# Optimization experiments

Measured on AMD Instinct MI355X. Metric: run time of the kernel, lower is better.

## Reference

```python
import jax, jax.numpy as jnp
import numpy as np

N = 4096     # batch of positions
E = 32       # descriptor buckets (experts)
NBLK = 12    # residual blocks per head


def _ln(x, g, b, eps=1e-5):
    m = x.mean(-1, keepdims=True)
    v = ((x - m) ** 2).mean(-1, keepdims=True)
    return (x - m) / jnp.sqrt(v + eps) * g + b


def _gelu(x):
    return jax.nn.gelu(x, approximate=False)  # torch nn.GELU default = exact erf


def setup_inputs() -> dict:
    key = jax.random.key(0)
    ks = iter(jax.random.split(key, 64))

    def nrm(shape, scale=0.05):
        return jax.random.normal(next(ks), shape, jnp.float32) * scale

    return {
        "piece_idx": jax.random.randint(next(ks), (N, 64), 0, 12),
        "side_flag": jax.random.randint(next(ks), (N,), 0, 2),
        "ep_file": jax.random.randint(next(ks), (N,), 0, 8),
        "castle_ms": jax.random.uniform(next(ks), (N, 4), jnp.float32),
        "fifty_a": jax.random.uniform(next(ks), (N,), jnp.float32),
        "descriptor_index": jax.random.randint(next(ks), (N,), 0, E),
        # per-bucket embedding tables, stacked on a leading expert axis
        "Wp_w": nrm((E, 64, 12, 32)), "Wp_b": nrm((E, 64, 12, 32)),
        "Wc_w": nrm((E, 4, 32)), "Wc_b": nrm((E, 4, 32)),
        "Wep_w": nrm((E, 8, 32)), "Wep_b": nrm((E, 8, 32)),
        "Wf_w": nrm((E, 2, 32)), "Wf_b": nrm((E, 2, 32)),
        # per-bucket MLP head params (weights stored as [in,out])
        "fc1_w": nrm((E, 2240, 256)), "fc1_b": nrm((E, 256)),
        "ln1_g": jnp.ones((E, 256)), "ln1_b": jnp.zeros((E, 256)),
        "fc2_w": nrm((E, 256, 32)), "fc2_b": nrm((E, 32)),
        "ln2_g": jnp.ones((E, 32)), "ln2_b": jnp.zeros((E, 32)),
        "blkA_w": nrm((NBLK, E, 32, 32)), "blkA_b": nrm((NBLK, E, 32)),
        "blkA_g": jnp.ones((NBLK, E, 32)), "blkA_be": jnp.zeros((NBLK, E, 32)),
        "blkB_w": nrm((NBLK, E, 32, 32)), "blkB_b": nrm((NBLK, E, 32)),
        "blkB_g": jnp.ones((NBLK, E, 32)), "blkB_be": jnp.zeros((NBLK, E, 32)),
        "out_w": nrm((E, 32, 51)), "out_b": nrm((E, 51)),
        "bins": jnp.linspace(0.0, 1.0, 51),
    }


def reference(piece_idx, side_flag, ep_file, castle_ms, fifty_a, descriptor_index,
              Wp_w, Wp_b, Wc_w, Wc_b, Wep_w, Wep_b, Wf_w, Wf_b,
              fc1_w, fc1_b, ln1_g, ln1_b, fc2_w, fc2_b, ln2_g, ln2_b,
              blkA_w, blkA_b, blkA_g, blkA_be, blkB_w, blkB_b, blkB_g, blkB_be,
              out_w, out_b, bins):
    desc = descriptor_index
    side = side_flag.astype(bool)
    n = piece_idx.shape[0]

    # ---- per-bucket, side-selected embedding gathers -> x_emb [N,2240] ----
    sq = jnp.arange(64)
    pc = jnp.maximum(piece_idx, 0)                                 # clamp -1 -> 0
    w_emb = Wp_w[desc[:, None], sq[None, :], pc]                    # [N,64,32]
    b_emb = Wp_b[desc[:, None], sq[None, :], pc]
    piece_emb = jnp.where(side[:, None, None], b_emb, w_emb)
    piece_emb = piece_emb * (piece_idx >= 0)[..., None].astype(piece_emb.dtype)
    pieces_vec = piece_emb.reshape(n, 2048)

    Wc = jnp.where(side[:, None, None], Wc_b[desc], Wc_w[desc])     # [N,4,32]
    castle_vec = (castle_ms[..., None] * Wc).reshape(n, 128)

    Wep = jnp.where(side[:, None, None], Wep_b[desc], Wep_w[desc])  # [N,8,32]
    epc = jnp.maximum(ep_file, 0)
    ep_vec = jnp.take_along_axis(Wep, epc[:, None, None], axis=1)[:, 0]
    ep_vec = ep_vec * (ep_file >= 0)[:, None].astype(ep_vec.dtype)

    Wf = jnp.where(side[:, None, None], Wf_b[desc], Wf_w[desc])     # [N,2,32]
    fifty_vec = (1.0 - fifty_a)[:, None] * Wf[:, 0] + fifty_a[:, None] * Wf[:, 1]

    x = jnp.concatenate([pieces_vec, castle_vec, ep_vec, fifty_vec], axis=1)  # [N,2240]

    # ---- expert-routed dense layer: all-expert GEMM + per-token select ----
    def dense_moe(h, W, b):
        ha = jnp.einsum('nd,edh->neh', h, W)                        # [N,E,out]
        hsel = jnp.take_along_axis(ha, desc[:, None, None], axis=1)[:, 0]
        return hsel + b[desc]

    h = _ln(_gelu(dense_moe(x, fc1_w, fc1_b)), ln1_g[desc], ln1_b[desc])   # [N,256]
    h = _ln(_gelu(dense_moe(h, fc2_w, fc2_b)), ln2_g[desc], ln2_b[desc])   # [N,32]

    def blk(carry, p):
        wA, bA, gA, beA, wB, bB, gB, beB = p
        y = _ln(_gelu(dense_moe(carry, wA, bA)), gA[desc], beA[desc])
        y = _ln(_gelu(dense_moe(y, wB, bB)), gB[desc], beB[desc])
        return carry + y, None

    h, _ = jax.lax.scan(blk, h, (blkA_w, blkA_b, blkA_g, blkA_be,
                                 blkB_w, blkB_b, blkB_g, blkB_be))

    logits = dense_moe(_gelu(h), out_w, out_b)                      # [N,51]
    p_win = jnp.sum(jax.nn.softmax(logits, axis=-1) * bins, axis=-1, keepdims=True)
    return logits, p_win
```

## Files before the change

### kernel.cpp

```cpp
#include <hip/hip_runtime.h>
#include <math.h>

#define N 4096
#define E 32
#define NBLK 12
#define D_IN 2240
#define H1 256
#define H2 32
#define NOUT 51
#define MT 16
#define NPAD (N + E*(MT-1))
#define NTILE (NPAD/MT)
#define KSPLIT 8
#define NROWS 4608
#define GMAX 96

typedef short s8v __attribute__((ext_vector_type(8)));
typedef float f4v __attribute__((ext_vector_type(4)));

__device__ __forceinline__ float gelu(float x){
    return 0.5f * x * (1.0f + erff(x * 0.70710678118654752f));
}
__device__ __forceinline__ unsigned short f2bf(float f){
    unsigned int u = __float_as_uint(f);
    unsigned int r = (u + 0x7fffu + ((u >> 16) & 1u)) >> 16;
    return (unsigned short)r;
}
__device__ __forceinline__ float bflo(unsigned int u){ return __uint_as_float(u << 16); }
__device__ __forceinline__ float bfhi(unsigned int u){ return __uint_as_float(u & 0xffff0000u); }

template<int CTRL>
__device__ __forceinline__ float dppadd(float x){
    int y = __builtin_amdgcn_update_dpp(0, __float_as_int(x), CTRL, 0xF, 0xF, true);
    return x + __int_as_float(y);
}
__device__ __forceinline__ float red32(float x){
    x = dppadd<0x121>(x);
    x = dppadd<0x122>(x);
    x = dppadd<0x124>(x);
    x = dppadd<0x128>(x);
    int y = __builtin_amdgcn_ds_swizzle(__float_as_int(x), 0x401F);
    return x + __int_as_float(y);
}

__global__ void k_pack(const float* __restrict__ W2,
                       const float* __restrict__ Aw, const float* __restrict__ Bw,
                       const int* __restrict__ desc_idx,
                       unsigned int* __restrict__ w2pk_g, unsigned int* __restrict__ rpk_g,
                       int* __restrict__ perm, int* __restrict__ tile_e,
                       int4* __restrict__ garr, int* __restrict__ ngroups){
    int tid = threadIdx.x;
    if (blockIdx.x == 2048){
        __shared__ int scnt[E];
        __shared__ int spoff[E+1];
        __shared__ int scur[E];
        if (tid < E) scnt[tid] = 0;
        __syncthreads();
        for (int n = tid; n < N; n += blockDim.x) atomicAdd(&scnt[desc_idx[n]], 1);
        __syncthreads();
        if (tid == 0){
            int run = 0;
            for (int e = 0; e < E; e++){ spoff[e] = run; run += ((scnt[e] + MT - 1)/MT)*MT; }
            spoff[E] = run;
            int ng = 0;
            for (int e = 0; e < E; e++){
                int t0 = spoff[e]/MT, t1 = spoff[e+1]/MT;
                for (int t = t0; t < t1; t += 8){
                    int nv = t1 - t; if (nv > 8) nv = 8;
                    if (ng < GMAX) garr[ng] = make_int4(t, e, nv, 0);
                    ng++;
                }
            }
            *ngroups = (ng > GMAX) ? GMAX : ng;
        }
        __syncthreads();
        if (tid < E) scur[tid] = spoff[tid];
        for (int p = tid; p < NPAD + 64; p += blockDim.x) perm[p] = -1;
        __syncthreads();
        for (int n = tid; n < N; n += blockDim.x){
            int p = atomicAdd(&scur[desc_idx[n]], 1);
            perm[p] = n;
        }
        for (int t = tid; t < NTILE; t += blockDim.x){
            int p0 = t*MT;
            int e = -1;
            if (p0 < spoff[E]){
                for (int q = 0; q < E; q++){
                    if (p0 >= spoff[q] && p0 < spoff[q+1]){ e = q; break; }
                }
            }
            tile_e[t] = e;
        }
        return;
    }
    int j = blockIdx.x*256 + tid;
    if (j < E*4096){
        int e = j >> 12, idx = j & 4095;
        int h = idx & 1, q = idx >> 1, cc = q & 31, p2 = q >> 5;
        int k0 = 4*p2 + 2*h;
        const float* W2e = W2 + (size_t)e*H1*H2;
        unsigned int lo = f2bf(W2e[k0*32 + cc]);
        unsigned int hi = f2bf(W2e[(k0+1)*32 + cc]);
        w2pk_g[((size_t)e << 12) + (p2*32 + cc)*2 + h] = lo | (hi << 16);
    } else {
        int i = j - E*4096;
        int slot = i & 511;
        int m = i >> 9;
        int e = m & 31, mat = m >> 5;
        int tb = mat >> 1, s = mat & 1;
        int h = slot & 1, q = slot >> 1, cc = q & 31, p2 = q >> 5;
        int k0 = 4*p2 + 2*h;
        const float* src = s ? Bw : Aw;
        size_t base = ((size_t)tb*E + e)*1024;
        unsigned int lo = f2bf(src[base + k0*32 + cc]);
        unsigned int hi = f2bf(src[base + (k0+1)*32 + cc]);
        rpk_g[((size_t)m << 9) + slot] = lo | (hi << 16);
    }
}

__global__ void k_prep(const int* __restrict__ perm,
                       const int* __restrict__ piece_idx,
                       const int* __restrict__ side_flag,
                       const int* __restrict__ ep_file,
                       const float* __restrict__ castle_ms,
                       const float* __restrict__ fifty_a,
                       const int* __restrict__ desc_idx,
                       const float* __restrict__ Wp_w, const float* __restrict__ Wp_b,
                       const float* __restrict__ Wc_w, const float* __restrict__ Wc_b,
                       const float* __restrict__ Wep_w, const float* __restrict__ Wep_b,
                       const float* __restrict__ Wf_w, const float* __restrict__ Wf_b,
                       unsigned short* __restrict__ xs){
    int tid = threadIdx.x;
    int pos = blockIdx.x;
    int row = perm[pos];
    unsigned short* xr = xs + (size_t)pos * D_IN;
    if (row < 0){
        s8v z = {0,0,0,0,0,0,0,0};
        for (int t = tid; t < D_IN/8; t += blockDim.x) *(s8v*)(xr + t*8) = z;
        return;
    }
    int d = desc_idx[row];
    int s = side_flag[row];
    __shared__ int pidx[64];
    if (tid < 64) pidx[tid] = piece_idx[row*64 + tid];
    __syncthreads();
    const float* Wp  = s ? Wp_b  : Wp_w;
    const float* Wc  = s ? Wc_b  : Wc_w;
    const float* Wep = s ? Wep_b : Wep_w;
    const float* Wf  = s ? Wf_b  : Wf_w;
    int ep  = ep_file[row];
    int epc = ep > 0 ? ep : 0;
    float a = fifty_a[row];
    for (int t = tid; t < D_IN/8; t += blockDim.x){
        int i0 = t*8;
        float v[8];
        if (i0 < 2048){
            int sq = i0 >> 5, c0 = i0 & 31;
            int pc = pidx[sq];
            float msk = pc >= 0 ? 1.0f : 0.0f;
            int pcc = pc > 0 ? pc : 0;
            const float* base = Wp + (((size_t)d*64 + sq)*12 + pcc)*32 + c0;
            float4 a0 = *(const float4*)base;
            float4 a1 = *(const float4*)(base + 4);
            v[0]=a0.x*msk; v[1]=a0.y*msk; v[2]=a0.z*msk; v[3]=a0.w*msk;
            v[4]=a1.x*msk; v[5]=a1.y*msk; v[6]=a1.z*msk; v[7]=a1.w*msk;
        } else if (i0 < 2176){
            int j = i0 - 2048; int ci = j >> 5, c0 = j & 31;
            float cv = castle_ms[row*4 + ci];
            const float* base = Wc + ((size_t)d*4 + ci)*32 + c0;
            float4 a0 = *(const float4*)base;
            float4 a1 = *(const float4*)(base + 4);
            v[0]=a0.x*cv; v[1]=a0.y*cv; v[2]=a0.z*cv; v[3]=a0.w*cv;
            v[4]=a1.x*cv; v[5]=a1.y*cv; v[6]=a1.z*cv; v[7]=a1.w*cv;
        } else if (i0 < 2208){
            int c0 = i0 - 2176;
            float msk = ep >= 0 ? 1.0f : 0.0f;
            const float* base = Wep + ((size_t)d*8 + epc)*32 + c0;
            float4 a0 = *(const float4*)base;
            float4 a1 = *(const float4*)(base + 4);
            v[0]=a0.x*msk; v[1]=a0.y*msk; v[2]=a0.z*msk; v[3]=a0.w*msk;
            v[4]=a1.x*msk; v[5]=a1.y*msk; v[6]=a1.z*msk; v[7]=a1.w*msk;
        } else {
            int c0 = i0 - 2208;
            #pragma unroll
            for (int j = 0; j < 8; j++)
                v[j] = (1.0f - a) * Wf[(size_t)d*64 + c0 + j] + a * Wf[(size_t)d*64 + 32 + c0 + j];
        }
        s8v p;
        #pragma unroll
        for (int j = 0; j < 8; j++) p[j] = (short)f2bf(v[j]);
        *(s8v*)(xr + i0) = p;
    }
}

__launch_bounds__(256)
__global__ void k_fc1(const int4* __restrict__ garr, const int* __restrict__ ngroups,
                      const unsigned short* __restrict__ xs,
                      const float* __restrict__ W1,
                      float* __restrict__ h1p){
    int g = blockIdx.x;
    if (g >= *ngroups) return;
    int4 gi = garr[g];
    int tile0 = gi.x, e = gi.y, nv = gi.z;
    int kc = blockIdx.y, nh = blockIdx.z;
    int kstart = (kc < 6) ? kc*9 : 54 + (kc-6)*8;
    int nsteps = (kc < 6) ? 9 : 8;
    int tid = threadIdx.x;
    int lane = tid & 63, wave = tid >> 6;
    int quad = lane >> 4, l16 = lane & 15;

    const unsigned short* Ab = xs + (size_t)(tile0*MT + l16)*D_IN + quad*8;

    const float* Bp = W1 + (size_t)e*D_IN*H1 + nh*128;
    int cl0 = wave*32 + l16;
    int cl1 = cl0 + 16;

    f4v acc[8][2];
    #pragma unroll
    for (int mt = 0; mt < 8; mt++){ acc[mt][0] = (f4v){0.f,0.f,0.f,0.f}; acc[mt][1] = (f4v){0.f,0.f,0.f,0.f}; }

    int kend = kstart + nsteps;
    for (int s = kstart; s < kend; s++){
        int kb = s*32;
        int krow = kb + quad*8;
        float b0f[8], b1f[8];
        #pragma unroll
        for (int j = 0; j < 8; j++){
            b0f[j] = Bp[(size_t)(krow + j)*H1 + cl0];
            b1f[j] = Bp[(size_t)(krow + j)*H1 + cl1];
        }
        s8v b0, b1;
        #pragma unroll
        for (int j = 0; j < 8; j++){
            b0[j] = (short)f2bf(b0f[j]);
            b1[j] = (short)f2bf(b1f[j]);
        }
        #pragma unroll
        for (int mt = 0; mt < 8; mt++){
            s8v av = *(const s8v*)(Ab + (size_t)mt*MT*D_IN + kb);
            acc[mt][0] = __builtin_amdgcn_mfma_f32_16x16x32_bf16(av, b0, acc[mt][0], 0, 0, 0);
            acc[mt][1] = __builtin_amdgcn_mfma_f32_16x16x32_bf16(av, b1, acc[mt][1], 0, 0, 0);
        }
    }
    int col0 = nh*128 + wave*32 + l16;
    float* out = h1p + (size_t)kc*NROWS*H1;
    #pragma unroll
    for (int mt = 0; mt < 8; mt++){
        if (mt >= nv) break;
        int posb = (tile0 + mt)*MT + quad*4;
        #pragma unroll
        for (int r = 0; r < 4; r++){
            out[(size_t)(posb + r)*H1 + col0]      = acc[mt][0][r];
            out[(size_t)(posb + r)*H1 + col0 + 16] = acc[mt][1][r];
        }
    }
}

__launch_bounds__(256)
__global__ void k_tail(const int* __restrict__ tile_e, const int* __restrict__ perm,
                       const float* __restrict__ h1p, const float* __restrict__ b1,
                       const float* __restrict__ g1, const float* __restrict__ be1,
                       const unsigned int* __restrict__ w2pk_g, const float* __restrict__ b2,
                       const float* __restrict__ g2, const float* __restrict__ be2,
                       const unsigned int* __restrict__ rpk,
                       const float* __restrict__ Abv, const float* __restrict__ Ag,
                       const float* __restrict__ Abe,
                       const float* __restrict__ Bb, const float* __restrict__ Bg,
                       const float* __restrict__ Bbe,
                       const float* __restrict__ Ow, const float* __restrict__ Ob,
                       const float* __restrict__ bins,
                       float* __restrict__ out){
    int th = blockIdx.x;
    int t  = th >> 1;
    int r0 = (th & 1) * 8;
    int e = tile_e[t];
    if (e < 0) return;
    int tid = threadIdx.x;

    __shared__ __align__(16) float        shf[8*260];
    __shared__ __align__(16) unsigned int W2pk[4096];
    __shared__ __align__(16) float        vecs[NBLK*6*32];
    __shared__ __align__(16) float        sh2[8][36];
    __shared__ __align__(16) float        sh3[8][36];

    {
        const unsigned int* src = w2pk_g + ((size_t)e << 12);
        for (int j = tid; j < 4096; j += 256) W2pk[j] = src[j];
    }
    for (int j = tid; j < NBLK*6*32; j += 256){
        int cc = j & 31, vi = (j >> 5) % 6, tb = j / 192;
        size_t wb = (size_t)tb*E + e;
        const float* src;
        switch(vi){ case 0: src=Abv; break; case 1: src=Ag; break; case 2: src=Abe; break;
                    case 3: src=Bb;  break; case 4: src=Bg; break; default: src=Bbe; }
        vecs[j] = src[wb*32 + cc];
    }
    #pragma unroll
    for (int it = 0; it < 2; it++){
        int slot = it*256 + tid;
        int r = slot >> 6, c4 = (slot & 63) << 2;
        int row = t*MT + r0 + r;
        float4 v = {0.f,0.f,0.f,0.f};
        #pragma unroll
        for (int kc = 0; kc < KSPLIT; kc++){
            float4 p = *(const float4*)(h1p + ((size_t)kc*NROWS + row)*H1 + c4);
            v.x += p.x; v.y += p.y; v.z += p.z; v.w += p.w;
        }
        float4 bb = *(const float4*)(b1 + e*H1 + c4);
        shf[r*260 + c4]   = gelu(v.x + bb.x);
        shf[r*260 + c4+1] = gelu(v.y + bb.y);
        shf[r*260 + c4+2] = gelu(v.z + bb.z);
        shf[r*260 + c4+3] = gelu(v.w + bb.w);
    }
    __syncthreads();

    int m = tid >> 5, c = tid & 31;
    {
        float s = 0.f, s2 = 0.f;
        #pragma unroll
        for (int j = 0; j < 8; j++){
            float x = shf[m*260 + c + 32*j];
            s += x; s2 += x*x;
        }
        s  = red32(s);
        s2 = red32(s2);
        float mean = s * (1.0f/H1);
        float var  = s2 * (1.0f/H1) - mean*mean;
        float rs = rsqrtf(var + 1e-5f);
        #pragma unroll
        for (int j = 0; j < 8; j++){
            int k = c + 32*j;
            shf[m*260 + k] = (shf[m*260 + k] - mean) * rs * g1[e*H1 + k] + be1[e*H1 + k];
        }
    }
    float hv;
    {
        const uint2* W2p = (const uint2*)W2pk;
        float q0=0.f,q1=0.f,q2=0.f,q3=0.f;
        #pragma unroll 8
        for (int p2 = 0; p2 < 64; p2++){
            uint2 w = W2p[p2*32 + c];
            float4 h4 = *(const float4*)(shf + m*260 + p2*4);
            q0 = fmaf(h4.x, bflo(w.x), q0);
            q1 = fmaf(h4.y, bfhi(w.x), q1);
            q2 = fmaf(h4.z, bflo(w.y), q2);
            q3 = fmaf(h4.w, bfhi(w.y), q3);
        }
        float acc = (q0+q1) + (q2+q3) + b2[e*H2 + c];
        float y = gelu(acc);
        float s  = red32(y);
        float s2 = red32(y*y);
        float mean2 = s * (1.0f/H2);
        float var2  = s2 * (1.0f/H2) - mean2*mean2;
        hv = (y - mean2) * rsqrtf(var2 + 1e-5f) * g2[e*H2+c] + be2[e*H2+c];
    }

    for (int tb = 0; tb < NBLK; tb++){
        const float* vA = &vecs[tb*192];
        const uint2* WA = (const uint2*)(rpk + (((size_t)(tb*2+0)*E + e) << 9));
        const uint2* WB = (const uint2*)(rpk + (((size_t)(tb*2+1)*E + e) << 9));
        sh2[m][c] = hv;
        float q0=0.f,q1=0.f,q2=0.f,q3=0.f;
        #pragma unroll
        for (int p2 = 0; p2 < 8; p2++){
            uint2 w = WA[p2*32 + c];
            float4 h4 = *(const float4*)(&sh2[m][p2*4]);
            q0 = fmaf(h4.x, bflo(w.x), q0);
            q1 = fmaf(h4.y, bfhi(w.x), q1);
            q2 = fmaf(h4.z, bflo(w.y), q2);
            q3 = fmaf(h4.w, bfhi(w.y), q3);
        }
        float ya = (q0+q1) + (q2+q3) + vA[c];
        ya = gelu(ya);
        float sa  = red32(ya);
        float sa2 = red32(ya*ya);
        float ma = sa * (1.0f/H2);
        float va = sa2 * (1.0f/H2) - ma*ma;
        float yA = (ya - ma) * rsqrtf(va + 1e-5f) * vA[32+c] + vA[64+c];
        sh3[m][c] = yA;
        q0=0.f; q1=0.f; q2=0.f; q3=0.f;
        #pragma unroll
        for (int p2 = 0; p2 < 8; p2++){
            uint2 w = WB[p2*32 + c];
            float4 h4 = *(const float4*)(&sh3[m][p2*4]);
            q0 = fmaf(h4.x, bflo(w.x), q0);
            q1 = fmaf(h4.y, bfhi(w.x), q1);
            q2 = fmaf(h4.z, bflo(w.y), q2);
            q3 = fmaf(h4.w, bfhi(w.y), q3);
        }
        float yb = (q0+q1) + (q2+q3) + vA[96+c];
        yb = gelu(yb);
        float sb  = red32(yb);
        float sb2 = red32(yb*yb);
        float mb = sb * (1.0f/H2);
        float vb = sb2 * (1.0f/H2) - mb*mb;
        hv += (yb - mb) * rsqrtf(vb + 1e-5f) * vA[128+c] + vA[160+c];
    }

    sh2[m][c] = gelu(hv);
    __syncthreads();
    int wave = tid >> 6, lane = tid & 63;
    const float* W = Ow + (size_t)e*32*NOUT;
    for (int rr = wave; rr < 8; rr += 4){
        int orow = perm[t*MT + r0 + rr];
        if (orow < 0) continue;
        float acc = (lane < NOUT) ? Ob[e*NOUT + lane] : -INFINITY;
        #pragma unroll
        for (int k = 0; k < 32; k++){
            float gk = sh2[rr][k];
            if (lane < NOUT) acc = fmaf(gk, W[k*NOUT + lane], acc);
        }
        if (lane < NOUT) out[(size_t)orow*NOUT + lane] = acc;
        float mx = acc;
        #pragma unroll
        for (int o = 32; o > 0; o >>= 1) mx = fmaxf(mx, __shfl_xor(mx, o));
        float pp = (lane < NOUT) ? expf(acc - mx) : 0.0f;
        float sum = pp;
        float pb = (lane < NOUT) ? pp * bins[lane] : 0.0f;
        float sb = pb;
        #pragma unroll
        for (int o = 32; o > 0; o >>= 1){ sum += __shfl_xor(sum, o); sb += __shfl_xor(sb, o); }
        if (lane == 0) out[(size_t)N*NOUT + orow] = sb / sum;
    }
}

extern "C" void kernel_launch(void* const* d_in, const int* in_sizes, int n_in,
                              void* d_out, int out_size, void* d_ws, size_t ws_size,
                              hipStream_t stream){
    const int*   piece_idx = (const int*)d_in[0];
    const int*   side_flag = (const int*)d_in[1];
    const int*   ep_file   = (const int*)d_in[2];
    const float* castle_ms = (const float*)d_in[3];
    const float* fifty_a   = (const float*)d_in[4];
    const int*   desc      = (const int*)d_in[5];
    const float* Wp_w  = (const float*)d_in[6];
    const float* Wp_b  = (const float*)d_in[7];
    const float* Wc_w  = (const float*)d_in[8];
    const float* Wc_b  = (const float*)d_in[9];
    const float* Wep_w = (const float*)d_in[10];
    const float* Wep_b = (const float*)d_in[11];
    const float* Wf_w  = (const float*)d_in[12];
    const float* Wf_b  = (const float*)d_in[13];
    const float* fc1_w = (const float*)d_in[14];
    const float* fc1_b = (const float*)d_in[15];
    const float* ln1_g = (const float*)d_in[16];
    const float* ln1_b = (const float*)d_in[17];
    const float* fc2_w = (const float*)d_in[18];
    const float* fc2_b = (const float*)d_in[19];
    const float* ln2_g = (const float*)d_in[20];
    const float* ln2_b = (const float*)d_in[21];
    const float* blkA_w  = (const float*)d_in[22];
    const float* blkA_b  = (const float*)d_in[23];
    const float* blkA_g  = (const float*)d_in[24];
    const float* blkA_be = (const float*)d_in[25];
    const float* blkB_w  = (const float*)d_in[26];
    const float* blkB_b  = (const float*)d_in[27];
    const float* blkB_g  = (const float*)d_in[28];
    const float* blkB_be = (const float*)d_in[29];
    const float* out_w = (const float*)d_in[30];
    const float* out_b = (const float*)d_in[31];
    const float* bins  = (const float*)d_in[32];

    char* wsp = (char*)d_ws;
    auto alloc = [&](size_t bytes){ void* p = (void*)wsp; wsp += (bytes + 255) & ~(size_t)255; return p; };
    int*            perm    = (int*)            alloc((size_t)(NPAD+128)*4);
    int*            tile_e  = (int*)            alloc((size_t)NTILE*4);
    int4*           garr    = (int4*)           alloc((size_t)GMAX*16);
    int*            ngroups = (int*)            alloc(256);
    unsigned int*   w2pk_g  = (unsigned int*)   alloc((size_t)E*4096*4);
    unsigned int*   rpk     = (unsigned int*)   alloc((size_t)24*E*512*4);
    unsigned short* xs      = (unsigned short*) alloc((size_t)(NPAD+128)*D_IN*2);
    float*          h1p     = (float*)          alloc((size_t)KSPLIT*NROWS*H1*4);

    k_pack<<<2049, 256, 0, stream>>>(fc2_w, blkA_w, blkB_w, desc,
                                     w2pk_g, rpk, perm, tile_e, garr, ngroups);
    k_prep<<<NPAD, 256, 0, stream>>>(perm, piece_idx, side_flag, ep_file,
                                     castle_ms, fifty_a, desc,
                                     Wp_w, Wp_b, Wc_w, Wc_b,
                                     Wep_w, Wep_b, Wf_w, Wf_b, xs);
    k_fc1<<<dim3(GMAX, KSPLIT, 2), 256, 0, stream>>>(garr, ngroups, xs, fc1_w, h1p);
    k_tail<<<NTILE*2, 256, 0, stream>>>(tile_e, perm, h1p, fc1_b, ln1_g, ln1_b,
                                        w2pk_g, fc2_b, ln2_g, ln2_b,
                                        rpk,
                                        blkA_b, blkA_g, blkA_be,
                                        blkB_b, blkB_g, blkB_be,
                                        out_w, out_b, bins, (float*)d_out);
}
```

Measured before the change: 296.6 us.

## Pre-transpose fc1 weights to bf16 K-contiguous layout inside prep kernel

Adds extra blocks to the prep kernel that convert fc1 weights from fp32 [K,N] into a bf16 [E,N,K] buffer through an LDS transpose. The fc1 GEMM then reads each B fragment as a single 16-byte vector load, replacing eight strided scalar fp32 loads plus per-step bf16 conversion, and its K loop is unrolled by two. The cost is a full pass over the 73 MB weight tensor each call (read fp32, write bf16), whereas the old code read each weight once per group using it.

After: 304.2 us. 1.03x slower.

```diff
diff --git a/kernel.cpp b/kernel.cpp
--- a/kernel.cpp
+++ b/kernel.cpp
@@ -14,6 +14,7 @@
 #define KSPLIT 8
 #define NROWS 4608
 #define GMAX 96
+#define NCONVBLK (35*4*E)
 
 typedef short s8v __attribute__((ext_vector_type(8)));
 typedef float f4v __attribute__((ext_vector_type(4)));
@@ -129,8 +130,38 @@
                        const float* __restrict__ Wc_w, const float* __restrict__ Wc_b,
                        const float* __restrict__ Wep_w, const float* __restrict__ Wep_b,
                        const float* __restrict__ Wf_w, const float* __restrict__ Wf_b,
-                       unsigned short* __restrict__ xs){
+                       unsigned short* __restrict__ xs,
+                       const float* __restrict__ W1, unsigned short* __restrict__ Wt){
+    __shared__ float lds[64][65];
     int tid = threadIdx.x;
+    if (blockIdx.x >= NPAD){
+        int b = blockIdx.x - NPAD;
+        int kt = b % 35;
+        int nt = (b / 35) & 3;
+        int e  = b / 140;
+        int k0 = kt*64, n0 = nt*64;
+        int kk = tid >> 4, nn = (tid & 15) * 4;
+        const float* src = W1 + ((size_t)e*D_IN + k0)*H1 + n0;
+        #pragma unroll
+        for (int r = 0; r < 4; r++){
+            float4 v = *(const float4*)(src + (size_t)(kk + r*16)*H1 + nn);
+            lds[kk + r*16][nn]   = v.x;
+            lds[kk + r*16][nn+1] = v.y;
+            lds[kk + r*16][nn+2] = v.z;
+            lds[kk + r*16][nn+3] = v.w;
+        }
+        __syncthreads();
+        int n = tid >> 2, kq = tid & 3;
+        s8v p0, p1;
+        #pragma unroll
+        for (int j = 0; j < 8; j++) p0[j] = (short)f2bf(lds[kq*16 + j][n]);
+        #pragma unroll
+        for (int j = 0; j < 8; j++) p1[j] = (short)f2bf(lds[kq*16 + 8 + j][n]);
+        unsigned short* dst = Wt + ((size_t)(e*H1 + n0 + n))*D_IN + k0 + kq*16;
+        *(s8v*)dst       = p0;
+        *(s8v*)(dst + 8) = p1;
+        return;
+    }
     int pos = blockIdx.x;
     int row = perm[pos];
     unsigned short* xr = xs + (size_t)pos * D_IN;
@@ -196,7 +227,7 @@
 __launch_bounds__(256)
 __global__ void k_fc1(const int4* __restrict__ garr, const int* __restrict__ ngroups,
                       const unsigned short* __restrict__ xs,
-                      const float* __restrict__ W1,
+                      const unsigned short* __restrict__ Wt,
                       float* __restrict__ h1p){
     int g = blockIdx.x;
     if (g >= *ngroups) return;
@@ -208,41 +239,29 @@
     int tid = threadIdx.x;
     int lane = tid & 63, wave = tid >> 6;
     int quad = lane >> 4, l16 = lane & 15;
+    int col0 = nh*128 + wave*32 + l16;
 
     const unsigned short* Ab = xs + (size_t)(tile0*MT + l16)*D_IN + quad*8;
-
-    const float* Bp = W1 + (size_t)e*D_IN*H1 + nh*128;
-    int cl0 = wave*32 + l16;
-    int cl1 = cl0 + 16;
+    const unsigned short* B0 = Wt + ((size_t)e*H1 + col0)*D_IN + quad*8;
+    const unsigned short* B1 = B0 + (size_t)16*D_IN;
 
     f4v acc[8][2];
     #pragma unroll
     for (int mt = 0; mt < 8; mt++){ acc[mt][0] = (f4v){0.f,0.f,0.f,0.f}; acc[mt][1] = (f4v){0.f,0.f,0.f,0.f}; }
 
     int kend = kstart + nsteps;
+    #pragma unroll 2
     for (int s = kstart; s < kend; s++){
-        int kb = s*32;
-        int krow = kb + quad*8;
-        float b0f[8], b1f[8];
-        #pragma unroll
-        for (int j = 0; j < 8; j++){
-            b0f[j] = Bp[(size_t)(krow + j)*H1 + cl0];
-            b1f[j] = Bp[(size_t)(krow + j)*H1 + cl1];
-        }
-        s8v b0, b1;
-        #pragma unroll
-        for (int j = 0; j < 8; j++){
-            b0[j] = (short)f2bf(b0f[j]);
-            b1[j] = (short)f2bf(b1f[j]);
-        }
+        int ko = s*32;
+        s8v b0 = *(const s8v*)(B0 + ko);
+        s8v b1 = *(const s8v*)(B1 + ko);
         #pragma unroll
         for (int mt = 0; mt < 8; mt++){
-            s8v av = *(const s8v*)(Ab + (size_t)mt*MT*D_IN + kb);
+            s8v av = *(const s8v*)(Ab + (size_t)mt*MT*D_IN + ko);
             acc[mt][0] = __builtin_amdgcn_mfma_f32_16x16x32_bf16(av, b0, acc[mt][0], 0, 0, 0);
             acc[mt][1] = __builtin_amdgcn_mfma_f32_16x16x32_bf16(av, b1, acc[mt][1], 0, 0, 0);
         }
     }
-    int col0 = nh*128 + wave*32 + l16;
     float* out = h1p + (size_t)kc*NROWS*H1;
     #pragma unroll
     for (int mt = 0; mt < 8; mt++){
@@ -469,16 +488,18 @@
     int*            ngroups = (int*)            alloc(256);
     unsigned int*   w2pk_g  = (unsigned int*)   alloc((size_t)E*4096*4);
     unsigned int*   rpk     = (unsigned int*)   alloc((size_t)24*E*512*4);
+    unsigned short* Wt      = (unsigned short*) alloc((size_t)E*H1*D_IN*2);
     unsigned short* xs      = (unsigned short*) alloc((size_t)(NPAD+128)*D_IN*2);
     float*          h1p     = (float*)          alloc((size_t)KSPLIT*NROWS*H1*4);
 
     k_pack<<<2049, 256, 0, stream>>>(fc2_w, blkA_w, blkB_w, desc,
                                      w2pk_g, rpk, perm, tile_e, garr, ngroups);
-    k_prep<<<NPAD, 256, 0, stream>>>(perm, piece_idx, side_flag, ep_file,
-                                     castle_ms, fifty_a, desc,
-                                     Wp_w, Wp_b, Wc_w, Wc_b,
-                                     Wep_w, Wep_b, Wf_w, Wf_b, xs);
-    k_fc1<<<dim3(GMAX, KSPLIT, 2), 256, 0, stream>>>(garr, ngroups, xs, fc1_w, h1p);
+    k_prep<<<NPAD + NCONVBLK, 256, 0, stream>>>(perm, piece_idx, side_flag, ep_file,
+                                                castle_ms, fifty_a, desc,
+                                                Wp_w, Wp_b, Wc_w, Wc_b,
+                                                Wep_w, Wep_b, Wf_w, Wf_b,
+                                                xs, fc1_w, Wt);
+    k_fc1<<<dim3(GMAX, KSPLIT, 2), 256, 0, stream>>>(garr, ngroups, xs, Wt, h1p);
     k_tail<<<NTILE*2, 256, 0, stream>>>(tile_e, perm, h1p, fc1_b, ln1_g, ln1_b,
                                         w2pk_g, fc2_b, ln2_g, ln2_b,
                                         rpk,
```
